# Kernel optimization log

Measured on AMD Instinct MI355X. Metric: run time of the kernel, lower is better.

## Reference

```python
import jax, jax.numpy as jnp
import numpy as np


def setup_inputs() -> dict:
    key = jax.random.key(0)
    k1, k2 = jax.random.split(key)
    BATCH, SLOTS = 64, 65536   # 64 ciphertexts, 2^16 CKKS slots each
    NUM_T = 16                 # number of BSGS diagonal transforms (shifts 2^0..2^15)
    x = jax.random.normal(k1, (BATCH, SLOTS), dtype=jnp.float32)
    diagonals = jax.random.normal(k2, (NUM_T, SLOTS), dtype=jnp.float32)
    return {"x": x, "diagonals": diagonals, "stride": 1, "reps": 1}


def reference(x, diagonals, stride, reps):
    """FHE BSGS conv-as-linear-transform: rotate / plaintext-multiply / accumulate.

    Mirrors LinearTransform.evaluate_transforms:
      for i: out += roll(x, -2**i * stride) * diagonals[i]
      (two rescales are scale-management no-ops numerically)
      final conv roll by slots // (2 * reps).
    """
    slots = x.shape[-1]
    num_t = diagonals.shape[0]
    # Vectorize the rotations: gather all shifted copies at once.
    # shift for transform i is -2**i * stride (roll left by 2**i*stride).
    shifts = (2 ** jnp.arange(num_t, dtype=jnp.int32)) * stride        # [T]
    base = jnp.arange(slots, dtype=jnp.int32)                          # [S]
    idx = (base[None, :] + shifts[:, None]) % slots                    # [T, S] roll(-s) gather
    rolled = x[:, idx]                                                 # [B, T, S]
    out = jnp.einsum('bts,ts->bs', rolled, diagonals)                  # accumulate products
    # final conv roll: roll(slots // (2*reps)) => shift right
    out = jnp.roll(out, slots // (2 * reps), axis=-1)
    return out
```

## Files before the change

### kernel.cpp

```cpp
#include <hip/hip_runtime.h>


#define SLOTS 65536
#define MASK  65535
#define NB    4

__device__ __forceinline__ float4 shfl4(const float4 v, int lsel) {
    return make_float4(__shfl(v.x, lsel, 64), __shfl(v.y, lsel, 64),
                       __shfl(v.z, lsel, 64), __shfl(v.w, lsel, 64));
}

__global__ __launch_bounds__(256) void bsgs_kernel(
    const float* __restrict__ x,
    const float* __restrict__ diag,
    float* __restrict__ out)
{
    const int bid  = blockIdx.x;
    const int y    = bid & 15;
    const int xidx = bid >> 4;
    const int j    = xidx * 1024 + threadIdx.x * 4;
    const int bg   = y * NB;
    const int lane = threadIdx.x & 63;

    float4 dreg[16];
#pragma unroll
    for (int t = 0; t < 16; ++t)
        dreg[t] = *(const float4*)(diag + t * SLOTS + j);

    float4 acc[NB];
#pragma unroll
    for (int b = 0; b < NB; ++b) acc[b] = make_float4(0.f, 0.f, 0.f, 0.f);

#pragma unroll
    for (int b = 0; b < NB; ++b) {
        const float* __restrict__ xr = x + (size_t)(bg + b) * SLOTS;

        const float4 vA = *(const float4*)(xr + j);
        const float4 vE = *(const float4*)(xr + ((j + 256) & MASK));
        float4 vd[7];
#pragma unroll
        for (int t = 9; t < 16; ++t)
            vd[t - 9] = *(const float4*)(xr + ((j + (1 << t)) & MASK));

        float4 w[6];
#pragma unroll
        for (int i = 0; i < 6; ++i) {
            const int k  = 1 << i;
            const int lp = lane + k;
            const int ls = lp & 63;
            const float4 a = shfl4(vA, ls);
            const float4 e = shfl4(vE, ls);
            const bool useA = lp < 64;
            w[i] = make_float4(useA ? a.x : e.x, useA ? a.y : e.y,
                               useA ? a.z : e.z, useA ? a.w : e.w);
        }

        acc[b].x += vA.y   * dreg[0].x + vA.z   * dreg[1].x;
        acc[b].y += vA.z   * dreg[0].y + vA.w   * dreg[1].y;
        acc[b].z += vA.w   * dreg[0].z + w[0].x * dreg[1].z;
        acc[b].w += w[0].x * dreg[0].w + w[0].y * dreg[1].w;

#pragma unroll
        for (int t = 2; t <= 7; ++t) {
            const float4 v = w[t - 2];
            acc[b].x += v.x * dreg[t].x; acc[b].y += v.y * dreg[t].y;
            acc[b].z += v.z * dreg[t].z; acc[b].w += v.w * dreg[t].w;
        }
        acc[b].x += vE.x * dreg[8].x; acc[b].y += vE.y * dreg[8].y;
        acc[b].z += vE.z * dreg[8].z; acc[b].w += vE.w * dreg[8].w;
#pragma unroll
        for (int t = 9; t < 16; ++t) {
            const float4 v = vd[t - 9];
            acc[b].x += v.x * dreg[t].x; acc[b].y += v.y * dreg[t].y;
            acc[b].z += v.z * dreg[t].z; acc[b].w += v.w * dreg[t].w;
        }
    }

#pragma unroll
    for (int b = 0; b < NB; ++b)
        *(float4*)(out + (size_t)(bg + b) * SLOTS + (j ^ 32768)) = acc[b];
}

extern "C" void kernel_launch(void* const* d_in, const int* in_sizes, int n_in,
                              void* d_out, int out_size, void* d_ws, size_t ws_size,
                              hipStream_t stream) {
    const float* x    = (const float*)d_in[0];
    const float* diag = (const float*)d_in[1];
    float* out        = (float*)d_out;

    bsgs_kernel<<<dim3(1024), dim3(256), 0, stream>>>(x, diag, out);
}
```

Before: 83.95 us.

## Reorder BSGS loops to stream diagonals per transform and cap registers for occupancy

Inverts the loop order so each diagonal is loaded once per transform and applied to all batch rows, instead of keeping all 16 diagonals in registers. The launch bounds now request 4 waves per SIMD. Both changes aim to cut register pressure and raise occupancy, which helps hide memory latency in this bandwidth-bound kernel. The cost is that loads are scattered through the computation rather than issued up front, which may reduce memory-level parallelism per thread.

```diff
diff --git a/kernel.cpp b/kernel.cpp
--- a/kernel.cpp
+++ b/kernel.cpp
@@ -10,7 +10,18 @@
                        __shfl(v.z, lsel, 64), __shfl(v.w, lsel, 64));
 }
 
-__global__ __launch_bounds__(256) void bsgs_kernel(
+__device__ __forceinline__ float4 window(const float4 vA, const float4 vE,
+                                         int lane, int k) {
+    const int lp = lane + k;
+    const int ls = lp & 63;
+    const float4 a = shfl4(vA, ls);
+    const float4 e = shfl4(vE, ls);
+    const bool useA = lp < 64;
+    return make_float4(useA ? a.x : e.x, useA ? a.y : e.y,
+                       useA ? a.z : e.z, useA ? a.w : e.w);
+}
+
+__global__ __launch_bounds__(256, 4) void bsgs_kernel(
     const float* __restrict__ x,
     const float* __restrict__ diag,
     float* __restrict__ out)
@@ -22,57 +33,72 @@
     const int bg   = y * NB;
     const int lane = threadIdx.x & 63;
 
-    float4 dreg[16];
-#pragma unroll
-    for (int t = 0; t < 16; ++t)
-        dreg[t] = *(const float4*)(diag + t * SLOTS + j);
-
     float4 acc[NB];
 #pragma unroll
     for (int b = 0; b < NB; ++b) acc[b] = make_float4(0.f, 0.f, 0.f, 0.f);
 
+    {
+        float4 vA[NB], vE[NB];
 #pragma unroll
-    for (int b = 0; b < NB; ++b) {
-        const float* __restrict__ xr = x + (size_t)(bg + b) * SLOTS;
-
-        const float4 vA = *(const float4*)(xr + j);
-        const float4 vE = *(const float4*)(xr + ((j + 256) & MASK));
-        float4 vd[7];
-#pragma unroll
-        for (int t = 9; t < 16; ++t)
-            vd[t - 9] = *(const float4*)(xr + ((j + (1 << t)) & MASK));
-
-        float4 w[6];
-#pragma unroll
-        for (int i = 0; i < 6; ++i) {
-            const int k  = 1 << i;
-            const int lp = lane + k;
-            const int ls = lp & 63;
-            const float4 a = shfl4(vA, ls);
-            const float4 e = shfl4(vE, ls);
-            const bool useA = lp < 64;
-            w[i] = make_float4(useA ? a.x : e.x, useA ? a.y : e.y,
-                               useA ? a.z : e.z, useA ? a.w : e.w);
+        for (int b = 0; b < NB; ++b) {
+            const float* __restrict__ xr = x + (size_t)(bg + b) * SLOTS;
+            vA[b] = *(const float4*)(xr + j);
+            vE[b] = *(const float4*)(xr + ((j + 256) & MASK));
         }
 
-        acc[b].x += vA.y   * dreg[0].x + vA.z   * dreg[1].x;
-        acc[b].y += vA.z   * dreg[0].y + vA.w   * dreg[1].y;
-        acc[b].z += vA.w   * dreg[0].z + w[0].x * dreg[1].z;
-        acc[b].w += w[0].x * dreg[0].w + w[0].y * dreg[1].w;
+        float4 w1[NB];
+#pragma unroll
+        for (int b = 0; b < NB; ++b) w1[b] = window(vA[b], vE[b], lane, 1);
+
+        {
+            const float4 d0 = *(const float4*)(diag + 0 * SLOTS + j);
+            const float4 d1 = *(const float4*)(diag + 1 * SLOTS + j);
+#pragma unroll
+            for (int b = 0; b < NB; ++b) {
+                acc[b].x += vA[b].y * d0.x + vA[b].z  * d1.x;
+                acc[b].y += vA[b].z * d0.y + vA[b].w  * d1.y;
+                acc[b].z += vA[b].w * d0.z + w1[b].x  * d1.z;
+                acc[b].w += w1[b].x * d0.w + w1[b].y  * d1.w;
+            }
+        }
+        {
+            const float4 d = *(const float4*)(diag + 2 * SLOTS + j);
+#pragma unroll
+            for (int b = 0; b < NB; ++b) {
+                acc[b].x += w1[b].x * d.x; acc[b].y += w1[b].y * d.y;
+                acc[b].z += w1[b].z * d.z; acc[b].w += w1[b].w * d.w;
+            }
+        }
+#pragma unroll
+        for (int t = 3; t <= 7; ++t) {
+            const float4 d = *(const float4*)(diag + t * SLOTS + j);
+            const int k = 1 << (t - 2);
+#pragma unroll
+            for (int b = 0; b < NB; ++b) {
+                const float4 v = window(vA[b], vE[b], lane, k);
+                acc[b].x += v.x * d.x; acc[b].y += v.y * d.y;
+                acc[b].z += v.z * d.z; acc[b].w += v.w * d.w;
+            }
+        }
+        {
+            const float4 d = *(const float4*)(diag + 8 * SLOTS + j);
+#pragma unroll
+            for (int b = 0; b < NB; ++b) {
+                acc[b].x += vE[b].x * d.x; acc[b].y += vE[b].y * d.y;
+                acc[b].z += vE[b].z * d.z; acc[b].w += vE[b].w * d.w;
+            }
+        }
+    }
 
 #pragma unroll
-        for (int t = 2; t <= 7; ++t) {
-            const float4 v = w[t - 2];
-            acc[b].x += v.x * dreg[t].x; acc[b].y += v.y * dreg[t].y;
-            acc[b].z += v.z * dreg[t].z; acc[b].w += v.w * dreg[t].w;
-        }
-        acc[b].x += vE.x * dreg[8].x; acc[b].y += vE.y * dreg[8].y;
-        acc[b].z += vE.z * dreg[8].z; acc[b].w += vE.w * dreg[8].w;
+    for (int t = 9; t < 16; ++t) {
+        const float4 d = *(const float4*)(diag + t * SLOTS + j);
+        const int off = (j + (1 << t)) & MASK;
 #pragma unroll
-        for (int t = 9; t < 16; ++t) {
-            const float4 v = vd[t - 9];
-            acc[b].x += v.x * dreg[t].x; acc[b].y += v.y * dreg[t].y;
-            acc[b].z += v.z * dreg[t].z; acc[b].w += v.w * dreg[t].w;
+        for (int b = 0; b < NB; ++b) {
+            const float4 v = *(const float4*)(x + (size_t)(bg + b) * SLOTS + off);
+            acc[b].x += v.x * d.x; acc[b].y += v.y * d.y;
+            acc[b].z += v.z * d.z; acc[b].w += v.w * d.w;
         }
     }
 
```

Result: slower. 86.06 us (+2.5%).

## Stage 2048-wide x strip in LDS and read short-shift rotations from shared memory

Applied to the files above, without the earlier changes.

Replaces the wavefront shuffle-based handling of shifts 1..256 with a shared-memory strip of 2048 floats per batch row, loaded cooperatively once per block. Shifts up to 1024 are then read from LDS, and only shifts 2048 and above are still fetched from global memory. This removes the many cross-lane shuffles and several global loads per batch row. The cost is a __syncthreads, 32KB of LDS per block that may limit occupancy, and possible LDS bank conflicts on the unaligned offsets.

```diff
diff --git a/kernel.cpp b/kernel.cpp
--- a/kernel.cpp
+++ b/kernel.cpp
@@ -4,28 +4,38 @@
 #define SLOTS 65536
 #define MASK  65535
 #define NB    4
-
-__device__ __forceinline__ float4 shfl4(const float4 v, int lsel) {
-    return make_float4(__shfl(v.x, lsel, 64), __shfl(v.y, lsel, 64),
-                       __shfl(v.z, lsel, 64), __shfl(v.w, lsel, 64));
-}
+#define STRIPW 2048
 
 __global__ __launch_bounds__(256) void bsgs_kernel(
     const float* __restrict__ x,
     const float* __restrict__ diag,
     float* __restrict__ out)
 {
+    __shared__ float sstrip[NB][STRIPW];
+
     const int bid  = blockIdx.x;
     const int y    = bid & 15;
     const int xidx = bid >> 4;
-    const int j    = xidx * 1024 + threadIdx.x * 4;
+    const int tid  = threadIdx.x;
+    const int J    = xidx * 1024;
+    const int j    = J + tid * 4;
     const int bg   = y * NB;
-    const int lane = threadIdx.x & 63;
 
     float4 dreg[16];
 #pragma unroll
     for (int t = 0; t < 16; ++t)
         dreg[t] = *(const float4*)(diag + t * SLOTS + j);
+
+#pragma unroll
+    for (int b = 0; b < NB; ++b) {
+        const float* __restrict__ xr = x + (size_t)(bg + b) * SLOTS;
+#pragma unroll
+        for (int h = 0; h < 2; ++h) {
+            const int i = tid * 4 + h * 1024;
+            *(float4*)(&sstrip[b][i]) = *(const float4*)(xr + ((J + i) & MASK));
+        }
+    }
+    __syncthreads();
 
     float4 acc[NB];
 #pragma unroll
@@ -35,42 +45,33 @@
     for (int b = 0; b < NB; ++b) {
         const float* __restrict__ xr = x + (size_t)(bg + b) * SLOTS;
 
-        const float4 vA = *(const float4*)(xr + j);
-        const float4 vE = *(const float4*)(xr + ((j + 256) & MASK));
-        float4 vd[7];
+        float4 vd[5];
 #pragma unroll
-        for (int t = 9; t < 16; ++t)
-            vd[t - 9] = *(const float4*)(xr + ((j + (1 << t)) & MASK));
+        for (int t = 11; t < 16; ++t)
+            vd[t - 11] = *(const float4*)(xr + ((j + (1 << t)) & MASK));
 
-        float4 w[6];
-#pragma unroll
-        for (int i = 0; i < 6; ++i) {
-            const int k  = 1 << i;
-            const int lp = lane + k;
-            const int ls = lp & 63;
-            const float4 a = shfl4(vA, ls);
-            const float4 e = shfl4(vE, ls);
-            const bool useA = lp < 64;
-            w[i] = make_float4(useA ? a.x : e.x, useA ? a.y : e.y,
-                               useA ? a.z : e.z, useA ? a.w : e.w);
-        }
+        const float* sp = &sstrip[b][tid * 4];
+        const float4 v0 = *(const float4*)(sp);
+        const float4 w4 = *(const float4*)(sp + 4);
 
-        acc[b].x += vA.y   * dreg[0].x + vA.z   * dreg[1].x;
-        acc[b].y += vA.z   * dreg[0].y + vA.w   * dreg[1].y;
-        acc[b].z += vA.w   * dreg[0].z + w[0].x * dreg[1].z;
-        acc[b].w += w[0].x * dreg[0].w + w[0].y * dreg[1].w;
+        acc[b].x += v0.y * dreg[0].x + v0.z * dreg[1].x;
+        acc[b].y += v0.z * dreg[0].y + v0.w * dreg[1].y;
+        acc[b].z += v0.w * dreg[0].z + w4.x * dreg[1].z;
+        acc[b].w += w4.x * dreg[0].w + w4.y * dreg[1].w;
+
+        acc[b].x += w4.x * dreg[2].x; acc[b].y += w4.y * dreg[2].y;
+        acc[b].z += w4.z * dreg[2].z; acc[b].w += w4.w * dreg[2].w;
 
 #pragma unroll
-        for (int t = 2; t <= 7; ++t) {
-            const float4 v = w[t - 2];
+        for (int t = 3; t <= 10; ++t) {
+            const float4 v = *(const float4*)(sp + (1 << t));
             acc[b].x += v.x * dreg[t].x; acc[b].y += v.y * dreg[t].y;
             acc[b].z += v.z * dreg[t].z; acc[b].w += v.w * dreg[t].w;
         }
-        acc[b].x += vE.x * dreg[8].x; acc[b].y += vE.y * dreg[8].y;
-        acc[b].z += vE.z * dreg[8].z; acc[b].w += vE.w * dreg[8].w;
+
 #pragma unroll
-        for (int t = 9; t < 16; ++t) {
-            const float4 v = vd[t - 9];
+        for (int t = 11; t < 16; ++t) {
+            const float4 v = vd[t - 11];
             acc[b].x += v.x * dreg[t].x; acc[b].y += v.y * dreg[t].y;
             acc[b].z += v.z * dreg[t].z; acc[b].w += v.w * dreg[t].w;
         }
```

Result: no change. 82.46 us (median of 2 runs) (-1.8%).
